# Optimization experiments

Hardware: AMD Instinct MI355X
Metric: run time of the kernel (lower is better)

## Reference

```python
import jax, jax.numpy as jnp
import numpy as np

DIM = 512
HEADS = 8
DIM_HEAD = 64
SCALE = DIM_HEAD ** -0.5


def setup_inputs() -> dict:
    key = jax.random.key(0)
    ks = jax.random.split(key, 4)
    b, n = 4, 2048
    x = jax.random.normal(ks[0], (b, n, DIM), dtype=jnp.float32)
    Wq = jax.random.normal(ks[1], (DIM, HEADS * DIM_HEAD), dtype=jnp.float32) * (DIM ** -0.5)
    Wkv = jax.random.normal(ks[2], (DIM, 2 * HEADS * DIM_HEAD), dtype=jnp.float32) * (DIM ** -0.5)
    Wo = jax.random.normal(ks[3], (HEADS * DIM_HEAD, DIM), dtype=jnp.float32) * ((HEADS * DIM_HEAD) ** -0.5)
    bo = jnp.zeros((DIM,), dtype=jnp.float32)
    return {"x": x, "Wq": Wq, "Wkv": Wkv, "Wo": Wo, "bo": bo}


def reference(x, Wq, Wkv, Wo, bo):
    b, n, _ = x.shape
    # context = x (self-attention path, kv_include_self=False)
    q = x @ Wq                      # [b, n, h*d]
    kv = x @ Wkv                    # [b, n, 2*h*d]
    k, v = jnp.split(kv, 2, axis=-1)

    def split_heads(t):
        return t.reshape(b, n, HEADS, DIM_HEAD).transpose(0, 2, 1, 3)  # [b,h,n,d]

    q, k, v = split_heads(q), split_heads(k), split_heads(v)
    dots = jnp.einsum('bhid,bhjd->bhij', q, k) * SCALE  # [b,h,n,n]
    attn = jax.nn.softmax(dots, axis=-1)
    out = jnp.einsum('bhij,bhjd->bhid', attn, v)        # [b,h,n,d]
    out = out.transpose(0, 2, 1, 3).reshape(b, n, HEADS * DIM_HEAD)
    return out @ Wo + bo
```

## Files before the change

kernel.cpp:

```cpp
#include <hip/hip_runtime.h>
#include <hip/hip_bf16.h>

typedef short bf16x8 __attribute__((ext_vector_type(8)));
typedef float fx4    __attribute__((ext_vector_type(4)));
typedef unsigned uint32x2 __attribute__((ext_vector_type(2)));

#if __has_builtin(__builtin_amdgcn_exp2f)
#define EXP2 __builtin_amdgcn_exp2f
#else
#define EXP2 exp2f
#endif

__device__ __forceinline__ unsigned pk2(float a, float b) {
  union { __hip_bfloat162 h; unsigned u; } cv;
  cv.h = __float22bfloat162_rn(float2{a, b});
  return cv.u;
}
__device__ __forceinline__ uint2 pk4(const fx4& v) {
  uint2 r;
  r.x = pk2(v[0], v[1]);
  r.y = pk2(v[2], v[3]);
  return r;
}

__device__ __forceinline__ void gld16(const void* g, void* l) {
  __builtin_amdgcn_global_load_lds(
      (const __attribute__((address_space(1))) unsigned int*)g,
      (__attribute__((address_space(3))) unsigned int*)l, 16, 0, 0);
}

__device__ __forceinline__ void bar_raw() {
  asm volatile("s_barrier" ::: "memory");
}
__device__ __forceinline__ void bar_lgkm() {
  asm volatile("s_waitcnt lgkmcnt(0)\ns_barrier" ::: "memory");
}
__device__ __forceinline__ void bar_lgkm_vm4() {
  asm volatile("s_waitcnt vmcnt(4) lgkmcnt(0)\ns_barrier" ::: "memory");
}
__device__ __forceinline__ void bar_vm_lgkm() {
  asm volatile("s_waitcnt vmcnt(0) lgkmcnt(0)\ns_barrier" ::: "memory");
}
__device__ __forceinline__ void cfence() { asm volatile("" ::: "memory"); }

__global__ __launch_bounds__(256) void prep_kernel(
    const float* __restrict__ x, const float* __restrict__ Wq,
    const float* __restrict__ Wkv, const float* __restrict__ Wo,
    short* __restrict__ xb, short* __restrict__ WallT, short* __restrict__ WoT,
    float qscale) {
  const int bx = blockIdx.x, tid = threadIdx.x;
  if (bx < 4096) {
    int i = bx * 256 + tid;
    const float4 s = *(const float4*)(x + (size_t)i * 4);
    uint2 o; o.x = pk2(s.x, s.y); o.y = pk2(s.z, s.w);
    *(uint2*)(xb + (size_t)i * 4) = o;
    return;
  }
  __shared__ float t[32][33];
  const int idx = bx - 4096;
  const int wb = idx & 63, kt = (idx >> 6) * 32;
  const bool mode0 = wb < 48;
  const int ct = (mode0 ? wb : wb - 48) * 32;
  const int tx = tid & 31, ty = tid >> 5;
  short* outT = mode0 ? WallT : WoT;
#pragma unroll
  for (int s = 0; s < 4; ++s) {
    int k = kt + ty + s * 8;
    int c = ct + tx;
    float v;
    if (mode0) v = (c < 512) ? Wq[(size_t)k * 512 + c] * qscale
                             : Wkv[(size_t)k * 1024 + (c - 512)];
    else       v = Wo[(size_t)k * 512 + c];
    t[ty + s * 8][tx] = v;
  }
  __syncthreads();
#pragma unroll
  for (int s = 0; s < 4; ++s) {
    int c = ct + ty + s * 8;
    int k = kt + tx;
    unsigned u = __float_as_uint(t[tx][ty + s * 8]);
    u = (u + 0x7fffu + ((u >> 16) & 1u)) >> 16;
    outT[(size_t)c * 512 + k] = (short)u;
  }
}

__global__ __launch_bounds__(256) void gemm_qkv(
    const short* __restrict__ A, const short* __restrict__ Bt,
    short* __restrict__ oq, short* __restrict__ ok, short* __restrict__ ovT) {
  __shared__ short As[2 * 128 * 32];
  __shared__ short Bs[2 * 128 * 32];
  const int K = 512;
  const int tid = threadIdx.x;
  const int wave = tid >> 6, lane = tid & 63;
  const int quad = lane >> 4, l15 = lane & 15;
  const int wm = wave >> 1, wn = wave & 1;
  const int blk = blockIdx.x;
  const int xcd = blk & 7, slot = blk >> 3;
  const int m0 = ((slot / 12) * 8 + xcd) * 128;
  const int n0 = (slot % 12) * 128;
  const bool swapped = (n0 < 1024);

  int arow[4], aoff[4];
#pragma unroll
  for (int c = 0; c < 4; ++c) {
    int u = c * 256 + tid;
    int slab = u >> 9, r2 = u & 511;
    arow[c] = r2 >> 2;
    aoff[c] = slab * 32 + (r2 & 3) * 8;
  }

  fx4 acc[4][4];
#pragma unroll
  for (int i = 0; i < 4; ++i)
#pragma unroll
    for (int j = 0; j < 4; ++j) acc[i][j] = fx4{0.f, 0.f, 0.f, 0.f};

  bf16x8 apre[4];
#pragma unroll
  for (int c = 0; c < 4; ++c)
    apre[c] = *(const bf16x8*)(A + (size_t)(m0 + arow[c]) * K + aoff[c]);

  for (int k0 = 0; k0 < K; k0 += 64) {
    bar_raw();
#pragma unroll
    for (int c = 0; c < 4; ++c)
      *(bf16x8*)(As + (size_t)(c * 256 + tid) * 8) = apre[c];
#pragma unroll
    for (int c = 0; c < 4; ++c) {
      int u = c * 256 + tid;
      int slab = u >> 9, r2 = u & 511;
      gld16(Bt + (size_t)(n0 + (r2 >> 2)) * K + k0 + slab * 32 + (r2 & 3) * 8,
            Bs + (size_t)(c * 256 + wave * 64) * 8);
    }
    cfence();
    {
      int kn = (k0 + 64) & 511;
#pragma unroll
      for (int c = 0; c < 4; ++c)
        apre[c] = *(const bf16x8*)(A + (size_t)(m0 + arow[c]) * K + kn + aoff[c]);
    }
    bar_lgkm_vm4();

#pragma unroll
    for (int ks2 = 0; ks2 < 2; ++ks2) {
      bf16x8 af[4], bfr[4];
#pragma unroll
      for (int i = 0; i < 4; ++i)
        af[i] = *(const bf16x8*)(As + ks2 * 4096 + (wm * 64 + i * 16 + l15) * 32 + quad * 8);
#pragma unroll
      for (int i = 0; i < 4; ++i)
        bfr[i] = *(const bf16x8*)(Bs + ks2 * 4096 + (wn * 64 + i * 16 + l15) * 32 + quad * 8);
      if (swapped) {
#pragma unroll
        for (int mi = 0; mi < 4; ++mi)
#pragma unroll
          for (int ni = 0; ni < 4; ++ni)
            acc[mi][ni] = __builtin_amdgcn_mfma_f32_16x16x32_bf16(bfr[ni], af[mi], acc[mi][ni], 0, 0, 0);
      } else {
#pragma unroll
        for (int mi = 0; mi < 4; ++mi)
#pragma unroll
          for (int ni = 0; ni < 4; ++ni)
            acc[mi][ni] = __builtin_amdgcn_mfma_f32_16x16x32_bf16(af[mi], bfr[ni], acc[mi][ni], 0, 0, 0);
      }
    }
  }

  const int rowb = m0 + wm * 64;
  const int colb = n0 + wn * 64;
  const int cls = n0 >> 9;
  if (cls < 2) {
    short* base = (cls == 0) ? oq : ok;
#pragma unroll
    for (int mi = 0; mi < 4; ++mi) {
      int t = rowb + mi * 16 + l15;
      int bb = t >> 11, ii = t & 2047;
#pragma unroll
      for (int ni = 0; ni < 4; ++ni) {
        int f = (colb + ni * 16 + quad * 4) & 511;
        int hh = f >> 6, dd = f & 63;
        *(uint2*)(base + ((size_t)(bb * 8 + hh) * 2048 + ii) * 64 + dd) = pk4(acc[mi][ni]);
      }
    }
  } else {
#pragma unroll
    for (int mi = 0; mi < 4; ++mi) {
      int rbase = rowb + mi * 16 + quad * 4;
      int bb = rbase >> 11;
      int ii = rbase & 2047;
#pragma unroll
      for (int ni = 0; ni < 4; ++ni) {
        int c = (colb + ni * 16 + l15) & 511;
        int hh = c >> 6, dd = c & 63;
        *(uint2*)(ovT + ((size_t)(bb * 8 + hh) * 64 + dd) * 2048 + ii) = pk4(acc[mi][ni]);
      }
    }
  }
}

__global__ __launch_bounds__(256) void gemm_out(
    const short* __restrict__ A, const short* __restrict__ Bt,
    float* __restrict__ of, const float* __restrict__ bias) {
  __shared__ short As[2 * 64 * 32];
  __shared__ short Bs[2 * 128 * 32];
  const int K = 512, N = 512;
  const int tid = threadIdx.x;
  const int wave = tid >> 6, lane = tid & 63;
  const int quad = lane >> 4, l15 = lane & 15;
  const int wm = wave >> 1, wn = wave & 1;
  const int m0 = blockIdx.y * 64, n0 = blockIdx.x * 128;

  int arow[2], aoff[2], brow[4], boff[4];
#pragma unroll
  for (int c = 0; c < 2; ++c) {
    int u = c * 256 + tid;
    int slab = u >> 8, r2 = u & 255;
    arow[c] = r2 >> 2; aoff[c] = slab * 32 + (r2 & 3) * 8;
  }
#pragma unroll
  for (int c = 0; c < 4; ++c) {
    int u = c * 256 + tid;
    int slab = u >> 9, r2 = u & 511;
    brow[c] = r2 >> 2; boff[c] = slab * 32 + (r2 & 3) * 8;
  }

  fx4 acc[2][4];
#pragma unroll
  for (int i = 0; i < 2; ++i)
#pragma unroll
    for (int j = 0; j < 4; ++j) acc[i][j] = fx4{0.f, 0.f, 0.f, 0.f};

  bf16x8 apre[2], bpre[4];
#pragma unroll
  for (int c = 0; c < 2; ++c)
    apre[c] = *(const bf16x8*)(A + (size_t)(m0 + arow[c]) * K + aoff[c]);
#pragma unroll
  for (int c = 0; c < 4; ++c)
    bpre[c] = *(const bf16x8*)(Bt + (size_t)(n0 + brow[c]) * K + boff[c]);

  for (int k0 = 0; k0 < K; k0 += 64) {
    bar_raw();
#pragma unroll
    for (int c = 0; c < 2; ++c)
      *(bf16x8*)(As + (size_t)(c * 256 + tid) * 8) = apre[c];
#pragma unroll
    for (int c = 0; c < 4; ++c)
      *(bf16x8*)(Bs + (size_t)(c * 256 + tid) * 8) = bpre[c];
    {
      int kn = (k0 + 64) & 511;
#pragma unroll
      for (int c = 0; c < 2; ++c)
        apre[c] = *(const bf16x8*)(A + (size_t)(m0 + arow[c]) * K + kn + aoff[c]);
#pragma unroll
      for (int c = 0; c < 4; ++c)
        bpre[c] = *(const bf16x8*)(Bt + (size_t)(n0 + brow[c]) * K + kn + boff[c]);
    }
    bar_lgkm();

#pragma unroll
    for (int ks2 = 0; ks2 < 2; ++ks2) {
      bf16x8 af[2], bfr[4];
#pragma unroll
      for (int i = 0; i < 2; ++i)
        af[i] = *(const bf16x8*)(As + ks2 * 2048 + (wm * 32 + i * 16 + l15) * 32 + quad * 8);
#pragma unroll
      for (int i = 0; i < 4; ++i)
        bfr[i] = *(const bf16x8*)(Bs + ks2 * 4096 + (wn * 64 + i * 16 + l15) * 32 + quad * 8);
#pragma unroll
      for (int mi = 0; mi < 2; ++mi)
#pragma unroll
        for (int ni = 0; ni < 4; ++ni)
          acc[mi][ni] = __builtin_amdgcn_mfma_f32_16x16x32_bf16(af[mi], bfr[ni], acc[mi][ni], 0, 0, 0);
    }
  }

  const int rowb = m0 + wm * 32;
  const int colb = n0 + wn * 64;
#pragma unroll
  for (int mi = 0; mi < 2; ++mi)
#pragma unroll
    for (int ni = 0; ni < 4; ++ni) {
      int cg = colb + ni * 16 + l15;
      float bv = bias[cg];
#pragma unroll
      for (int r = 0; r < 4; ++r) {
        int rg = rowb + mi * 16 + quad * 4 + r;
        of[(size_t)rg * N + cg] = acc[mi][ni][r] + bv;
      }
    }
}

__global__ __launch_bounds__(256) void attn_kernel(
    const short* __restrict__ Q, const short* __restrict__ K,
    const short* __restrict__ Vt, short* __restrict__ O) {
  __shared__ short Ks[2 * 64 * 64];
  __shared__ short Vs[2 * 64 * 64];

  const int tid = threadIdx.x;
  const int wave = tid >> 6, lane = tid & 63;
  const int quad = lane >> 4, l15 = lane & 15;
  const int blk = blockIdx.x;
  const int xcd = blk & 7, slot = blk >> 3;
  const int bh = (slot >> 4) * 8 + xcd;
  const int qt = slot & 15;
  const int b = bh >> 3, h = bh & 7;
  const int i0 = qt * 128 + wave * 32;

  const int idx0 = tid, idx1 = 256 + tid;
  const int row0 = idx0 >> 3, sg0 = (idx0 & 7) ^ (row0 & 7);
  const int row1 = idx1 >> 3, sg1 = (idx1 & 7) ^ (row1 & 7);
  const short* Kb = K + (size_t)bh * 2048 * 64;
  const short* Vb = Vt + (size_t)bh * 64 * 2048;

  bf16x8 qf[2][2];
#pragma unroll
  for (int it = 0; it < 2; ++it)
#pragma unroll
    for (int ks = 0; ks < 2; ++ks)
      qf[it][ks] = *(const bf16x8*)(Q + ((size_t)bh * 2048 + i0 + it * 16 + l15) * 64 + ks * 32 + quad * 8);

  bf16x8 ones;
#pragma unroll
  for (int c = 0; c < 8; ++c) ones[c] = (short)0x3F80;

  fx4 oacc[2][4];
  fx4 acc_l[2] = { fx4{0.f,0.f,0.f,0.f}, fx4{0.f,0.f,0.f,0.f} };
#pragma unroll
  for (int it = 0; it < 2; ++it)
#pragma unroll
    for (int dt = 0; dt < 4; ++dt) oacc[it][dt] = fx4{0.f, 0.f, 0.f, 0.f};

  gld16(Kb + (size_t)row0 * 64 + sg0 * 8, Ks + wave * 512);
  gld16(Kb + (size_t)row1 * 64 + sg1 * 8, Ks + 2048 + wave * 512);
  gld16(Vb + (size_t)row0 * 2048 + sg0 * 8, Vs + wave * 512);
  gld16(Vb + (size_t)row1 * 2048 + sg1 * 8, Vs + 2048 + wave * 512);

  for (int j0 = 0; j0 < 2048; j0 += 64) {
    const int cur = (j0 >> 6) & 1;
    bar_vm_lgkm();
    if (j0 + 64 < 2048) {
      const int jn = j0 + 64;
      const int nb = (cur ^ 1) * 4096;
      gld16(Kb + (size_t)(jn + row0) * 64 + sg0 * 8, Ks + nb + wave * 512);
      gld16(Kb + (size_t)(jn + row1) * 64 + sg1 * 8, Ks + nb + 2048 + wave * 512);
      gld16(Vb + (size_t)row0 * 2048 + jn + sg0 * 8, Vs + nb + wave * 512);
      gld16(Vb + (size_t)row1 * 2048 + jn + sg1 * 8, Vs + nb + 2048 + wave * 512);
    }
    const short* Kc = Ks + cur * 4096;
    const short* Vc = Vs + cur * 4096;

    fx4 s[2][4];
#pragma unroll
    for (int it = 0; it < 2; ++it)
#pragma unroll
      for (int jt = 0; jt < 4; ++jt) s[it][jt] = fx4{0.f, 0.f, 0.f, 0.f};
    __builtin_amdgcn_s_setprio(1);
#pragma unroll
    for (int ks = 0; ks < 2; ++ks) {
#pragma unroll
      for (int jt = 0; jt < 4; ++jt) {
        bf16x8 kf = *(const bf16x8*)(Kc + (jt * 16 + l15) * 64 + (((ks * 4 + quad) ^ (l15 & 7)) * 8));
#pragma unroll
        for (int it = 0; it < 2; ++it)
          s[it][jt] = __builtin_amdgcn_mfma_f32_16x16x32_bf16(kf, qf[it][ks], s[it][jt], 0, 0, 0);
      }
    }
    __builtin_amdgcn_s_setprio(0);

    bf16x8 pfr[2][2];
#pragma unroll
    for (int it = 0; it < 2; ++it) {
      unsigned W[4][2];
#pragma unroll
      for (int jt = 0; jt < 4; ++jt) {
#pragma unroll
        for (int r = 0; r < 4; ++r) s[it][jt][r] = EXP2(s[it][jt][r]);
        W[jt][0] = pk2(s[it][jt][0], s[it][jt][1]);
        W[jt][1] = pk2(s[it][jt][2], s[it][jt][3]);
      }
#pragma unroll
      for (int k = 0; k < 2; ++k) {
        union { unsigned u[4]; bf16x8 v; } pw;
#pragma unroll
        for (int hh = 0; hh < 2; ++hh) {
          uint32x2 a = __builtin_amdgcn_permlane32_swap(W[2 * k][hh], W[2 * k + 1][hh], false, false);
          uint32x2 t = __builtin_amdgcn_permlane16_swap(a[0], a[1], false, false);
          pw.u[hh] = t[0];
          pw.u[2 + hh] = t[1];
        }
        pfr[it][k] = pw.v;
      }
    }

    __builtin_amdgcn_s_setprio(1);
#pragma unroll
    for (int kj = 0; kj < 2; ++kj) {
#pragma unroll
      for (int it = 0; it < 2; ++it)
        acc_l[it] = __builtin_amdgcn_mfma_f32_16x16x32_bf16(ones, pfr[it][kj], acc_l[it], 0, 0, 0);
#pragma unroll
      for (int dt = 0; dt < 4; ++dt) {
        bf16x8 vf = *(const bf16x8*)(Vc + (dt * 16 + l15) * 64 + (((kj * 4 + quad) ^ (l15 & 7)) * 8));
#pragma unroll
        for (int it = 0; it < 2; ++it)
          oacc[it][dt] = __builtin_amdgcn_mfma_f32_16x16x32_bf16(vf, pfr[it][kj], oacc[it][dt], 0, 0, 0);
      }
    }
    __builtin_amdgcn_s_setprio(0);
  }

#pragma unroll
  for (int it = 0; it < 2; ++it) {
    float inv = __builtin_amdgcn_rcpf(acc_l[it][0]);
    size_t rowbase = ((size_t)b * 2048 + i0 + it * 16 + l15) * 512 + h * 64;
#pragma unroll
    for (int dt = 0; dt < 4; ++dt) {
      fx4 o = oacc[it][dt] * inv;
      *(uint2*)(O + rowbase + dt * 16 + quad * 4) = pk4(o);
    }
  }
}

extern "C" void kernel_launch(void* const* d_in, const int* in_sizes, int n_in,
                              void* d_out, int out_size, void* d_ws, size_t ws_size,
                              hipStream_t stream) {
  const float* x   = (const float*)d_in[0];
  const float* Wq  = (const float*)d_in[1];
  const float* Wkv = (const float*)d_in[2];
  const float* Wo  = (const float*)d_in[3];
  const float* bo  = (const float*)d_in[4];
  float* out = (float*)d_out;

  char* p = (char*)d_ws;
  short* xb    = (short*)p; p += (size_t)8192 * 512 * 2;
  short* WallT = (short*)p; p += (size_t)1536 * 512 * 2;
  short* WoT   = (short*)p; p += (size_t)512 * 512 * 2;
  short* qb    = (short*)p; p += (size_t)32 * 2048 * 64 * 2;
  short* kb    = (short*)p; p += (size_t)32 * 2048 * 64 * 2;
  short* vTb   = (short*)p; p += (size_t)32 * 64 * 2048 * 2;
  short* Ob    = (short*)p; p += (size_t)8192 * 512 * 2;

  const float qscale = 0.125f * 1.4426950408889634f;

  prep_kernel<<<5120, 256, 0, stream>>>(x, Wq, Wkv, Wo, xb, WallT, WoT, qscale);
  gemm_qkv<<<768, 256, 0, stream>>>(xb, WallT, qb, kb, vTb);
  attn_kernel<<<512, 256, 0, stream>>>(qb, kb, vTb, Ob);
  gemm_out<<<dim3(4, 128), 256, 0, stream>>>(Ob, WoT, out, bo);
}
```

Baseline: 165.8 us.

## Software-pipeline attention loop: overlap next tile QK with current softmax-PV

Restructures the attention inner loop into a two-stage software pipeline: the QK^T MFMAs and V fragment loads for tile t+1 are issued before the exp/permute/PV work for tile t, using ping-pong score and V-fragment registers. The aim is to hide the exp and permlane latency behind independent MFMAs and to fuse the row-sum and PV MFMAs per packed fragment. It also adds an occupancy hint of 2 blocks per CU and drops the setprio calls. The extra live registers (two score and V fragment sets) risk spills or lower occupancy.

```diff
diff --git a/kernel.cpp b/kernel.cpp
--- a/kernel.cpp
+++ b/kernel.cpp
@@ -290,7 +290,7 @@
     }
 }
 
-__global__ __launch_bounds__(256) void attn_kernel(
+__global__ __launch_bounds__(256, 2) void attn_kernel(
     const short* __restrict__ Q, const short* __restrict__ K,
     const short* __restrict__ Vt, short* __restrict__ O) {
   __shared__ short Ks[2 * 64 * 64];
@@ -330,31 +330,19 @@
 #pragma unroll
     for (int dt = 0; dt < 4; ++dt) oacc[it][dt] = fx4{0.f, 0.f, 0.f, 0.f};
 
-  gld16(Kb + (size_t)row0 * 64 + sg0 * 8, Ks + wave * 512);
-  gld16(Kb + (size_t)row1 * 64 + sg1 * 8, Ks + 2048 + wave * 512);
-  gld16(Vb + (size_t)row0 * 2048 + sg0 * 8, Vs + wave * 512);
-  gld16(Vb + (size_t)row1 * 2048 + sg1 * 8, Vs + 2048 + wave * 512);
-
-  for (int j0 = 0; j0 < 2048; j0 += 64) {
-    const int cur = (j0 >> 6) & 1;
-    bar_vm_lgkm();
-    if (j0 + 64 < 2048) {
-      const int jn = j0 + 64;
-      const int nb = (cur ^ 1) * 4096;
-      gld16(Kb + (size_t)(jn + row0) * 64 + sg0 * 8, Ks + nb + wave * 512);
-      gld16(Kb + (size_t)(jn + row1) * 64 + sg1 * 8, Ks + nb + 2048 + wave * 512);
-      gld16(Vb + (size_t)row0 * 2048 + jn + sg0 * 8, Vs + nb + wave * 512);
-      gld16(Vb + (size_t)row1 * 2048 + jn + sg1 * 8, Vs + nb + 2048 + wave * 512);
-    }
-    const short* Kc = Ks + cur * 4096;
-    const short* Vc = Vs + cur * 4096;
-
-    fx4 s[2][4];
+  auto DMA = [&](int jn, int bufsel) {
+    const int nb = bufsel * 4096;
+    gld16(Kb + (size_t)(jn + row0) * 64 + sg0 * 8, Ks + nb + wave * 512);
+    gld16(Kb + (size_t)(jn + row1) * 64 + sg1 * 8, Ks + nb + 2048 + wave * 512);
+    gld16(Vb + (size_t)row0 * 2048 + jn + sg0 * 8, Vs + nb + wave * 512);
+    gld16(Vb + (size_t)row1 * 2048 + jn + sg1 * 8, Vs + nb + 2048 + wave * 512);
+  };
+
+  auto QK = [&](const short* Kc, fx4 (&s)[2][4]) {
 #pragma unroll
     for (int it = 0; it < 2; ++it)
 #pragma unroll
       for (int jt = 0; jt < 4; ++jt) s[it][jt] = fx4{0.f, 0.f, 0.f, 0.f};
-    __builtin_amdgcn_s_setprio(1);
 #pragma unroll
     for (int ks = 0; ks < 2; ++ks) {
 #pragma unroll
@@ -365,9 +353,17 @@
           s[it][jt] = __builtin_amdgcn_mfma_f32_16x16x32_bf16(kf, qf[it][ks], s[it][jt], 0, 0, 0);
       }
     }
-    __builtin_amdgcn_s_setprio(0);
-
-    bf16x8 pfr[2][2];
+  };
+
+  auto VLOAD = [&](const short* Vc, bf16x8 (&vf)[2][4]) {
+#pragma unroll
+    for (int kj = 0; kj < 2; ++kj)
+#pragma unroll
+      for (int dt = 0; dt < 4; ++dt)
+        vf[kj][dt] = *(const bf16x8*)(Vc + (dt * 16 + l15) * 64 + (((kj * 4 + quad) ^ (l15 & 7)) * 8));
+  };
+
+  auto SMPV = [&](fx4 (&s)[2][4], bf16x8 (&vf)[2][4]) {
 #pragma unroll
     for (int it = 0; it < 2; ++it) {
       unsigned W[4][2];
@@ -388,26 +384,41 @@
           pw.u[hh] = t[0];
           pw.u[2 + hh] = t[1];
         }
-        pfr[it][k] = pw.v;
-      }
-    }
-
-    __builtin_amdgcn_s_setprio(1);
-#pragma unroll
-    for (int kj = 0; kj < 2; ++kj) {
-#pragma unroll
-      for (int it = 0; it < 2; ++it)
-        acc_l[it] = __builtin_amdgcn_mfma_f32_16x16x32_bf16(ones, pfr[it][kj], acc_l[it], 0, 0, 0);
-#pragma unroll
-      for (int dt = 0; dt < 4; ++dt) {
-        bf16x8 vf = *(const bf16x8*)(Vc + (dt * 16 + l15) * 64 + (((kj * 4 + quad) ^ (l15 & 7)) * 8));
-#pragma unroll
-        for (int it = 0; it < 2; ++it)
-          oacc[it][dt] = __builtin_amdgcn_mfma_f32_16x16x32_bf16(vf, pfr[it][kj], oacc[it][dt], 0, 0, 0);
-      }
-    }
-    __builtin_amdgcn_s_setprio(0);
-  }
+        acc_l[it] = __builtin_amdgcn_mfma_f32_16x16x32_bf16(ones, pw.v, acc_l[it], 0, 0, 0);
+#pragma unroll
+        for (int dt = 0; dt < 4; ++dt)
+          oacc[it][dt] = __builtin_amdgcn_mfma_f32_16x16x32_bf16(vf[k][dt], pw.v, oacc[it][dt], 0, 0, 0);
+      }
+    }
+  };
+
+  fx4 sA[2][4], sB[2][4];
+  bf16x8 vfA[2][4], vfB[2][4];
+
+  DMA(0, 0);
+  bar_vm_lgkm();
+  DMA(64, 1);
+  QK(Ks, sA);
+  VLOAD(Vs, vfA);
+
+  for (int t1 = 1; t1 <= 29; t1 += 2) {
+    bar_vm_lgkm();
+    DMA((t1 + 1) << 6, 0);
+    QK(Ks + 4096, sB);
+    VLOAD(Vs + 4096, vfB);
+    SMPV(sA, vfA);
+    bar_vm_lgkm();
+    DMA((t1 + 2) << 6, 1);
+    QK(Ks, sA);
+    VLOAD(Vs, vfA);
+    SMPV(sB, vfB);
+  }
+
+  bar_vm_lgkm();
+  QK(Ks + 4096, sB);
+  VLOAD(Vs + 4096, vfB);
+  SMPV(sA, vfA);
+  SMPV(sB, vfB);
 
 #pragma unroll
   for (int it = 0; it < 2; ++it) {
```

Result: faster. 156.4 us (-5.6%).
